# Performance work log

Measured on AMD Instinct MI355X. Metric: run time of the kernel, lower is better.

Reference implementation:

```python
import jax, jax.numpy as jnp
import numpy as np

N_NODES = 50000
N_HEDGES = 20000
N_EDGES = 800000
D = 128
H = 4


def setup_inputs() -> dict:
    key = jax.random.key(0)
    ks = jax.random.split(key, 12)
    s = 1.0 / np.sqrt(D)
    return {
        "x_node": jax.random.normal(ks[0], (N_NODES, D), jnp.float32),
        "x_edge": jax.random.normal(ks[1], (N_HEDGES, D), jnp.float32),
        "src": jax.random.randint(ks[2], (N_EDGES,), 0, N_NODES, jnp.int32),
        "dst": jax.random.randint(ks[3], (N_EDGES,), 0, N_HEDGES, jnp.int32),
        "Wq": jax.random.normal(ks[4], (D, D), jnp.float32) * s,
        "bq": jnp.zeros((D,), jnp.float32),
        "Wk": jax.random.normal(ks[5], (D, D), jnp.float32) * s,
        "bk": jnp.zeros((D,), jnp.float32),
        "Wv": jax.random.normal(ks[6], (D, D), jnp.float32) * s,
        "bv": jnp.zeros((D,), jnp.float32),
        "Wo": jax.random.normal(ks[7], (D, D), jnp.float32) * s,
        "bo": jnp.zeros((D,), jnp.float32),
    }


def reference(x_node, x_edge, src, dst, Wq, bq, Wk, bk, Wv, bv, Wo, bo):
    N = x_node.shape[0]
    hd = Wq.shape[1] // H  # head_dim = 32
    Q = (x_node @ Wq + bq).reshape(N, H, hd)
    K = (x_edge @ Wk + bk).reshape(-1, H, hd)
    V = (x_edge @ Wv + bv).reshape(-1, H, hd)
    # per-edge gather: [E, H, hd]
    Qe = Q[src]
    Ke = K[dst]
    Ve = V[dst]
    # per-edge, per-head scores: [E, H]
    scores = jnp.einsum("ehd,ehd->eh", Qe, Ke) / jnp.sqrt(jnp.float32(hd))
    # segment softmax grouped by src node
    m = jax.ops.segment_max(scores, src, num_segments=N)  # [N, H]
    e = jnp.exp(scores - m[src])
    z = jax.ops.segment_sum(e, src, num_segments=N)  # [N, H]
    w = e / z[src]  # [E, H]
    # weighted scatter-add of V messages back to src nodes
    msg = w[:, :, None] * Ve  # [E, H, hd]
    out = jax.ops.segment_sum(msg, src, num_segments=N)  # [N, H, hd]
    out = out.reshape(N, -1)
    return out @ Wo + bo + x_node
```

## Files before the change

kernel.cpp:

```cpp
#include <hip/hip_runtime.h>

#define D 128
#define STRIDE 6144

typedef _Float16 f16;
typedef f16 f16x2 __attribute__((ext_vector_type(2)));
typedef f16 f16x8 __attribute__((ext_vector_type(8)));
typedef float f32x4 __attribute__((ext_vector_type(4)));

__device__ inline f16x2 u2h(unsigned u) { return __builtin_bit_cast(f16x2, u); }
__device__ inline unsigned h2u(f16x2 h) { return __builtin_bit_cast(unsigned, h); }

__device__ inline float dot2(unsigned a, unsigned b, float c) {
#if __has_builtin(__builtin_amdgcn_fdot2)
    return __builtin_amdgcn_fdot2(u2h(a), u2h(b), c, false);
#else
    f16x2 x = u2h(a), y = u2h(b);
    return c + (float)x.x * (float)y.x + (float)x.y * (float)y.y;
#endif
}

__global__ void wt_prep4(const float* __restrict__ W0, const float* __restrict__ W1,
                         const float* __restrict__ W2, const float* __restrict__ W3,
                         f16* __restrict__ Wt) {
    const float* W = (blockIdx.x == 0) ? W0 : (blockIdx.x == 1) ? W1 : (blockIdx.x == 2) ? W2 : W3;
    f16* o = Wt + (size_t)blockIdx.x * D * D;
    int t = threadIdx.x;
#pragma unroll
    for (int i = 0; i < 16; ++i) {
        int f = t + i * 256;
        int k = f >> 5, c4 = f & 31;
        float4 v = *(const float4*)(W + k * D + 4 * c4);
        float vv[4] = {v.x, v.y, v.z, v.w};
#pragma unroll
        for (int e = 0; e < 4; ++e) {
            int c = 4 * c4 + e;
            o[c * D + (((k >> 3) ^ (c & 15)) << 3) + (k & 7)] = (f16)vv[e];
        }
    }
}

__device__ inline void stage_w(const f16* __restrict__ Wt, f16* Wl, int t) {
#pragma unroll
    for (int i = 0; i < 8; ++i) ((uint4*)Wl)[t + i * 256] = ((const uint4*)Wt)[t + i * 256];
}

__device__ inline void stage_x_f32(const float* __restrict__ x, f16* xs, int r0, int nrows, int t) {
#pragma unroll
    for (int i = 0; i < 8; ++i) {
        int f = t + i * 256;
        int r = f >> 5, c4 = f & 31;
        int gr = r0 + r;
        float4 v = {0.f, 0.f, 0.f, 0.f};
        if (gr < nrows) v = *(const float4*)(x + (size_t)gr * D + 4 * c4);
        unsigned lo = h2u((f16x2){(f16)v.x, (f16)v.y});
        unsigned hi = h2u((f16x2){(f16)v.z, (f16)v.w});
        *(uint2*)(xs + r * D + (((c4 >> 1) ^ (r & 15)) << 3) + (c4 & 1) * 4) = (uint2){lo, hi};
    }
}

__device__ inline void mfma_core(const f16* xs, const f16* Wl, f32x4 acc[8], int lane, int w) {
    int lr = lane & 15, g = lane >> 4;
    int arow = 16 * w + lr;
#pragma unroll
    for (int kc = 0; kc < 4; ++kc) {
        int slot = kc * 4 + g;
        f16x8 af = *(const f16x8*)(xs + arow * D + ((slot ^ (arow & 15)) << 3));
#pragma unroll
        for (int ct = 0; ct < 8; ++ct) {
            int col = ct * 16 + lr;
            f16x8 bf = *(const f16x8*)(Wl + col * D + ((slot ^ (col & 15)) << 3));
            acc[ct] = __builtin_amdgcn_mfma_f32_16x16x32_f16(af, bf, acc[ct], 0, 0, 0);
        }
    }
}

__global__ __launch_bounds__(256) void fused_front(
    const float* __restrict__ x_node, const float* __restrict__ x_edge,
    const int* __restrict__ src, const int* __restrict__ dst,
    const f16* __restrict__ Wt,
    const float* __restrict__ bq, const float* __restrict__ bk, const float* __restrict__ bv,
    f16* __restrict__ Qh, f16* __restrict__ KVh,
    int* __restrict__ bucket_cnt, unsigned* __restrict__ temp,
    int N, int M, int E, int nsp, int nq, float qscale) {
    __shared__ __align__(16) f16 Wl[D * D];
    __shared__ __align__(16) f16 xs[64 * D];
    int t = threadIdx.x;
    int bid = blockIdx.x;

    if (bid < nsp) {
        int* hist = (int*)Wl;
        int* lex = hist + 256;
        int* gbase = lex + 256;
        int* lcur = gbase + 256;
        int* wsum = lcur + 256;
        int* sorted = wsum + 16;
        unsigned char* sbyte = (unsigned char*)xs;
        hist[t] = 0;
        lcur[t] = 0;
        __syncthreads();
        int base0 = bid * 4096;
        int lim = E - base0; if (lim > 4096) lim = 4096;
        for (int i = t; i < lim; i += 256) atomicAdd(&hist[src[base0 + i] >> 8], 1);
        __syncthreads();
        int v = hist[t];
        int inc = v;
#pragma unroll
        for (int m = 1; m < 64; m <<= 1) {
            int u = __shfl_up(inc, m);
            if ((t & 63) >= m) inc += u;
        }
        if ((t & 63) == 63) wsum[t >> 6] = inc;
        __syncthreads();
        int add = 0;
#pragma unroll
        for (int w = 0; w < 4; ++w)
            if (w < (t >> 6)) add += wsum[w];
        lex[t] = add + inc - v;
        if (v) gbase[t] = atomicAdd(&bucket_cnt[t], v);
        __syncthreads();
        for (int i = t; i < lim; i += 256) {
            int s = src[base0 + i];
            int bk2 = s >> 8;
            int lp = atomicAdd(&lcur[bk2], 1);
            int sp = lex[bk2] + lp;
            sorted[sp] = ((s & 255) << 24) | dst[base0 + i];
            sbyte[sp] = (unsigned char)bk2;
        }
        __syncthreads();
        for (int i = t; i < lim; i += 256) {
            int bk2 = sbyte[i];
            int gp = gbase[bk2] + (i - lex[bk2]);
            if (gp < STRIDE) temp[(size_t)bk2 * STRIDE + gp] = (unsigned)sorted[i];
        }
    } else if (bid < nsp + nq) {
        int r0 = (bid - nsp) * 64;
        stage_w(Wt, Wl, t);
        stage_x_f32(x_node, xs, r0, N, t);
        __syncthreads();
        int lane = t & 63, w = t >> 6;
        f32x4 acc[8];
#pragma unroll
        for (int i = 0; i < 8; ++i) acc[i] = (f32x4){0.f, 0.f, 0.f, 0.f};
        mfma_core(xs, Wl, acc, lane, w);
        __syncthreads();
        int lr = lane & 15, g = lane >> 4;
#pragma unroll
        for (int ct = 0; ct < 8; ++ct) {
            int col = ct * 16 + lr;
            float bias = bq[col];
#pragma unroll
            for (int rg = 0; rg < 4; ++rg) {
                int row = 16 * w + 4 * g + rg;
                xs[row * D + (((col >> 3) ^ (row & 15)) << 3) + (col & 7)] =
                    (f16)((acc[ct][rg] + bias) * qscale);
            }
        }
        __syncthreads();
#pragma unroll
        for (int i = 0; i < 4; ++i) {
            int f = t + i * 256;
            int r = f >> 4, c8 = f & 15;
            if (r0 + r < N) {
                uint4 v = *(const uint4*)(xs + r * D + ((c8 ^ (r & 15)) << 3));
                *(uint4*)(Qh + (size_t)(r0 + r) * D + 8 * c8) = v;
            }
        }
    } else {
        int r0 = (bid - nsp - nq) * 64;
        stage_w(Wt + D * D, Wl, t);
        stage_x_f32(x_edge, xs, r0, M, t);
        __syncthreads();
        int lane = t & 63, w = t >> 6;
        f32x4 accK[8], accV[8];
#pragma unroll
        for (int i = 0; i < 8; ++i) accK[i] = accV[i] = (f32x4){0.f, 0.f, 0.f, 0.f};
        mfma_core(xs, Wl, accK, lane, w);
        __syncthreads();
        stage_w(Wt + 2 * D * D, Wl, t);
        __syncthreads();
        mfma_core(xs, Wl, accV, lane, w);
        __syncthreads();
        int lr = lane & 15, g = lane >> 4;
#pragma unroll
        for (int ct = 0; ct < 8; ++ct) {
            int col = ct * 16 + lr;
            float bbk = bk[col], bbv = bv[col];
            int s = col >> 2, wk = col & 3;
#pragma unroll
            for (int rg = 0; rg < 4; ++rg) {
                int row = 16 * w + 4 * g + rg;
                f16* base = Wl + row * 256 + ((s ^ (row & 15)) << 3);
                base[wk] = (f16)(accK[ct][rg] + bbk);
                base[4 + wk] = (f16)(accV[ct][rg] + bbv);
            }
        }
        __syncthreads();
#pragma unroll
        for (int i = 0; i < 8; ++i) {
            int f = t + i * 256;
            int r = f >> 5, c8 = f & 31;
            if (r0 + r < M) {
                uint4 v = *(const uint4*)(Wl + r * 256 + ((c8 ^ (r & 15)) << 3));
                *(uint4*)(KVh + (size_t)(r0 + r) * 256 + 8 * c8) = v;
            }
        }
    }
}

__global__ __launch_bounds__(256) void bucket_scatter(const unsigned* __restrict__ temp,
                                                      const int* __restrict__ bucket_cnt,
                                                      int* __restrict__ off,
                                                      int* __restrict__ csr_dst,
                                                      int N, int E, int NBUK) {
    __shared__ int nh[256], cur[256], wsum[4], sc_ex[256];
    __shared__ int lds_dst[STRIDE];
    int b = blockIdx.x, t = threadIdx.x;
    int bc = (t < NBUK) ? bucket_cnt[t] : 0;
    {
        int inc = bc;
#pragma unroll
        for (int m = 1; m < 64; m <<= 1) {
            int u = __shfl_up(inc, m);
            if ((t & 63) >= m) inc += u;
        }
        if ((t & 63) == 63) wsum[t >> 6] = inc;
        __syncthreads();
        int add = 0;
#pragma unroll
        for (int w = 0; w < 4; ++w)
            if (w < (t >> 6)) add += wsum[w];
        sc_ex[t] = add + inc - bc;
        nh[t] = 0;
    }
    __syncthreads();
    int bo = sc_ex[b];
    int cnt = bucket_cnt[b];
    if (cnt > STRIDE) cnt = STRIDE;
    const unsigned* tb = temp + (size_t)b * STRIDE;
    for (int i = t; i < cnt; i += 256) atomicAdd(&nh[tb[i] >> 24], 1);
    __syncthreads();
    int v = nh[t];
    int inc = v;
#pragma unroll
    for (int m = 1; m < 64; m <<= 1) {
        int u = __shfl_up(inc, m);
        if ((t & 63) >= m) inc += u;
    }
    if ((t & 63) == 63) wsum[t >> 6] = inc;
    __syncthreads();
    int add = 0;
#pragma unroll
    for (int w = 0; w < 4; ++w)
        if (w < (t >> 6)) add += wsum[w];
    int ex = add + inc - v;
    cur[t] = ex;
    int node = (b << 8) + t;
    if (node < N) off[node] = bo + ex;
    if (b == 0 && t == 0) off[N] = E;
    __syncthreads();
    for (int i = t; i < cnt; i += 256) {
        unsigned it = tb[i];
        int lpos = atomicAdd(&cur[it >> 24], 1);
        lds_dst[lpos] = (int)(it & 0xFFFFFFu);
    }
    __syncthreads();
    for (int i = t; i < cnt; i += 256) csr_dst[bo + i] = lds_dst[i];
}

__global__ __launch_bounds__(256) void node_attn4(const f16* __restrict__ Qh,
                                                  const f16* __restrict__ KVh,
                                                  const int* __restrict__ off,
                                                  const int* __restrict__ csr,
                                                  f16* __restrict__ aggh, int N) {
    int wid = (int)((blockIdx.x * (size_t)blockDim.x + threadIdx.x) >> 6);
    int lane = threadIdx.x & 63;
    if (wid >= N) return;
    int j = lane & 7, g = lane >> 3;
    const f16* qp = Qh + (size_t)wid * D + 16 * j;
    uint4 qA = *(const uint4*)qp;
    uint4 qB = *(const uint4*)(qp + 8);
    int beg = off[wid], end = off[wid + 1];
    float z = 0.f;
    f16x2 a0 = {0, 0}, a1 = {0, 0}, a2 = {0, 0}, a3 = {0, 0};
    f16x2 a4 = {0, 0}, a5 = {0, 0}, a6 = {0, 0}, a7 = {0, 0};
    if (beg < end) {
        int pe = beg + g;
        int d0 = csr[(pe < end) ? pe : end - 1];
        const f16* r = KVh + (size_t)d0 * 256 + 32 * j;
        uint4 A0 = *(const uint4*)r;
        uint4 A1 = *(const uint4*)(r + 8);
        uint4 A2 = *(const uint4*)(r + 16);
        uint4 A3 = *(const uint4*)(r + 24);
        for (int p = beg; p < end; p += 8) {
            int pn = p + 8 + g;
            int dn = csr[(pn < end) ? pn : end - 1];
            const f16* rn = KVh + (size_t)dn * 256 + 32 * j;
            uint4 B0 = *(const uint4*)rn;
            uint4 B1 = *(const uint4*)(rn + 8);
            uint4 B2 = *(const uint4*)(rn + 16);
            uint4 B3 = *(const uint4*)(rn + 24);
            bool valid = (p + g) < end;
            float s = dot2(A0.x, qA.x, 0.f);
            s = dot2(A0.y, qA.y, s);
            s = dot2(A1.x, qA.z, s);
            s = dot2(A1.y, qA.w, s);
            s = dot2(A2.x, qB.x, s);
            s = dot2(A2.y, qB.y, s);
            s = dot2(A3.x, qB.z, s);
            s = dot2(A3.y, qB.w, s);
            s += __shfl_xor(s, 1);
            float eh = valid ? __expf(s) : 0.f;
            z += eh;
            f16 e16 = (f16)eh;
            f16x2 e2 = {e16, e16};
            a0 += e2 * u2h(A0.z); a1 += e2 * u2h(A0.w);
            a2 += e2 * u2h(A1.z); a3 += e2 * u2h(A1.w);
            a4 += e2 * u2h(A2.z); a5 += e2 * u2h(A2.w);
            a6 += e2 * u2h(A3.z); a7 += e2 * u2h(A3.w);
            A0 = B0; A1 = B1; A2 = B2; A3 = B3;
        }
    }
#pragma unroll
    for (int m = 8; m < 64; m <<= 1) {
        z += __shfl_xor(z, m);
        a0 += u2h(__shfl_xor((int)h2u(a0), m));
        a1 += u2h(__shfl_xor((int)h2u(a1), m));
        a2 += u2h(__shfl_xor((int)h2u(a2), m));
        a3 += u2h(__shfl_xor((int)h2u(a3), m));
        a4 += u2h(__shfl_xor((int)h2u(a4), m));
        a5 += u2h(__shfl_xor((int)h2u(a5), m));
        a6 += u2h(__shfl_xor((int)h2u(a6), m));
        a7 += u2h(__shfl_xor((int)h2u(a7), m));
    }
    if (g == 0) {
        float inv = (end > beg) ? 1.f / z : 0.f;
        uint4 o0, o1;
        o0.x = h2u((f16x2){(f16)((float)a0.x * inv), (f16)((float)a0.y * inv)});
        o0.y = h2u((f16x2){(f16)((float)a1.x * inv), (f16)((float)a1.y * inv)});
        o0.z = h2u((f16x2){(f16)((float)a2.x * inv), (f16)((float)a2.y * inv)});
        o0.w = h2u((f16x2){(f16)((float)a3.x * inv), (f16)((float)a3.y * inv)});
        o1.x = h2u((f16x2){(f16)((float)a4.x * inv), (f16)((float)a4.y * inv)});
        o1.y = h2u((f16x2){(f16)((float)a5.x * inv), (f16)((float)a5.y * inv)});
        o1.z = h2u((f16x2){(f16)((float)a6.x * inv), (f16)((float)a6.y * inv)});
        o1.w = h2u((f16x2){(f16)((float)a7.x * inv), (f16)((float)a7.y * inv)});
        f16* op = aggh + (size_t)wid * D + 16 * j;
        *(uint4*)op = o0;
        *(uint4*)(op + 8) = o1;
    }
}

__global__ __launch_bounds__(256) void gemm_o(const f16* __restrict__ aggh,
                                              const f16* __restrict__ Wt,
                                              const float* __restrict__ b,
                                              const float* __restrict__ resid,
                                              float* __restrict__ y, int nrows) {
    __shared__ __align__(16) f16 Wl[D * D];
    __shared__ __align__(16) f16 xs[64 * D];
    int t = threadIdx.x;
    int r0 = blockIdx.x * 64;
    stage_w(Wt, Wl, t);
#pragma unroll
    for (int i = 0; i < 4; ++i) {
        int f = t + i * 256;
        int r = f >> 4, c8 = f & 15;
        int gr = r0 + r;
        uint4 v = {0u, 0u, 0u, 0u};
        if (gr < nrows) v = *(const uint4*)(aggh + (size_t)gr * D + 8 * c8);
        *(uint4*)(xs + r * D + ((c8 ^ (r & 15)) << 3)) = v;
    }
    __syncthreads();
    int lane = t & 63, w = t >> 6;
    f32x4 acc[8];
#pragma unroll
    for (int i = 0; i < 8; ++i) acc[i] = (f32x4){0.f, 0.f, 0.f, 0.f};
    mfma_core(xs, Wl, acc, lane, w);
    __syncthreads();
    float* Tf = (float*)Wl;
    int lr = lane & 15, g = lane >> 4;
#pragma unroll
    for (int ct = 0; ct < 8; ++ct) {
        int col = ct * 16 + lr;
        float bias = b[col];
        int s = col >> 2, wk = col & 3;
#pragma unroll
        for (int rg = 0; rg < 4; ++rg) {
            int row = 16 * w + 4 * g + rg;
            Tf[row * D + ((s ^ (row & 15)) << 2) + wk] = acc[ct][rg] + bias;
        }
    }
    __syncthreads();
#pragma unroll
    for (int i = 0; i < 8; ++i) {
        int f = t + i * 256;
        int r = f >> 5, c4 = f & 31;
        int gr = r0 + r;
        if (gr < nrows) {
            float4 v = *(const float4*)(Tf + r * D + ((c4 ^ (r & 15)) << 2));
            float4 rv = *(const float4*)(resid + (size_t)gr * D + 4 * c4);
            v.x += rv.x; v.y += rv.y; v.z += rv.z; v.w += rv.w;
            *(float4*)(y + (size_t)gr * D + 4 * c4) = v;
        }
    }
}

extern "C" void kernel_launch(void* const* d_in, const int* in_sizes, int n_in,
                              void* d_out, int out_size, void* d_ws, size_t ws_size,
                              hipStream_t stream) {
    const float* x_node = (const float*)d_in[0];
    const float* x_edge = (const float*)d_in[1];
    const int* src = (const int*)d_in[2];
    const int* dst = (const int*)d_in[3];
    const float* Wq = (const float*)d_in[4];
    const float* bq = (const float*)d_in[5];
    const float* Wk = (const float*)d_in[6];
    const float* bk = (const float*)d_in[7];
    const float* Wv = (const float*)d_in[8];
    const float* bv = (const float*)d_in[9];
    const float* Wo = (const float*)d_in[10];
    const float* bo = (const float*)d_in[11];

    int N = in_sizes[0] / D;
    int M = in_sizes[1] / D;
    int E = in_sizes[2];
    int NBUK = (N + 255) >> 8;

    char* p = (char*)d_ws;
    auto alloc = [&](size_t bytes) -> char* {
        char* r = p;
        p += (bytes + 15) & ~(size_t)15;
        return r;
    };
    f16* Wt = (f16*)alloc((size_t)4 * D * D * 2);
    f16* Qh = (f16*)alloc((size_t)N * D * 2);
    f16* KVh = (f16*)alloc((size_t)M * 256 * 2);
    f16* aggh = (f16*)alloc((size_t)N * D * 2);
    int* bucket_cnt = (int*)alloc(256 * 4);
    int* off = (int*)alloc((size_t)(N + 1) * 4);
    unsigned* temp = (unsigned*)alloc((size_t)NBUK * STRIDE * 4);
    int* csr_dst = (int*)alloc((size_t)E * 4);
    float* out = (float*)d_out;

    hipMemsetAsync(bucket_cnt, 0, 256 * 4, stream);

    wt_prep4<<<4, 256, 0, stream>>>(Wq, Wk, Wv, Wo, Wt);

    int nq = (N + 63) / 64;
    int nkv = (M + 63) / 64;
    int nsp = (E + 4095) / 4096;
    fused_front<<<nsp + nq + nkv, 256, 0, stream>>>(x_node, x_edge, src, dst, Wt,
                                                    bq, bk, bv, Qh, KVh,
                                                    bucket_cnt, temp,
                                                    N, M, E, nsp, nq, 0.17677669529663687f);

    bucket_scatter<<<NBUK, 256, 0, stream>>>(temp, bucket_cnt, off, csr_dst, N, E, NBUK);

    int ablk = (int)(((size_t)N * 64 + 255) / 256);
    node_attn4<<<ablk, 256, 0, stream>>>(Qh, KVh, off, csr_dst, aggh, N);

    gemm_o<<<(N + 63) / 64, 256, 0, stream>>>(aggh, Wt + 3 * D * D, bo, x_node, out, N);
}
```

Measured before the change: 116.3 us.

## Load GEMM A-operands straight to registers and pre-sort buckets by dst

The GEMM kernels (fused_front Q/KV paths and gemm_o) now load their A-operand rows from global memory directly into MFMA register fragments, dropping the 16 KB xs LDS tile and its staging barrier. This halves shared memory per block, which should allow more resident blocks, and lets the global loads overlap the weight staging. The CSR build kernel adds a counting-sort pass by dst/128 before the per-node sort, so each node's edge list comes out grouped by destination locality, which should improve K/V gather cache hits in the attention kernel. The cost is an extra histogram, scan and scatter pass plus 24 KB more LDS in that kernel.

Result: faster. 114.0 us (-2.0%).

```diff
diff --git a/kernel.cpp b/kernel.cpp
--- a/kernel.cpp
+++ b/kernel.cpp
@@ -45,32 +45,33 @@
     for (int i = 0; i < 8; ++i) ((uint4*)Wl)[t + i * 256] = ((const uint4*)Wt)[t + i * 256];
 }
 
-__device__ inline void stage_x_f32(const float* __restrict__ x, f16* xs, int r0, int nrows, int t) {
-#pragma unroll
-    for (int i = 0; i < 8; ++i) {
-        int f = t + i * 256;
-        int r = f >> 5, c4 = f & 31;
-        int gr = r0 + r;
-        float4 v = {0.f, 0.f, 0.f, 0.f};
-        if (gr < nrows) v = *(const float4*)(x + (size_t)gr * D + 4 * c4);
-        unsigned lo = h2u((f16x2){(f16)v.x, (f16)v.y});
-        unsigned hi = h2u((f16x2){(f16)v.z, (f16)v.w});
-        *(uint2*)(xs + r * D + (((c4 >> 1) ^ (r & 15)) << 3) + (c4 & 1) * 4) = (uint2){lo, hi};
-    }
-}
-
-__device__ inline void mfma_core(const f16* xs, const f16* Wl, f32x4 acc[8], int lane, int w) {
+__device__ inline void load_a_f32(const float* __restrict__ x, int gr, int nrows, int g,
+                                  f16x8 a[4]) {
+#pragma unroll
+    for (int kc = 0; kc < 4; ++kc) {
+        float4 v0 = {0.f, 0.f, 0.f, 0.f}, v1 = {0.f, 0.f, 0.f, 0.f};
+        if (gr < nrows) {
+            const float* xr = x + (size_t)gr * D + (kc * 4 + g) * 8;
+            v0 = *(const float4*)xr;
+            v1 = *(const float4*)(xr + 4);
+        }
+        f16x8 af;
+        af[0] = (f16)v0.x; af[1] = (f16)v0.y; af[2] = (f16)v0.z; af[3] = (f16)v0.w;
+        af[4] = (f16)v1.x; af[5] = (f16)v1.y; af[6] = (f16)v1.z; af[7] = (f16)v1.w;
+        a[kc] = af;
+    }
+}
+
+__device__ inline void mfma_ra(const f16x8 a[4], const f16* Wl, f32x4 acc[8], int lane) {
     int lr = lane & 15, g = lane >> 4;
-    int arow = 16 * w + lr;
 #pragma unroll
     for (int kc = 0; kc < 4; ++kc) {
         int slot = kc * 4 + g;
-        f16x8 af = *(const f16x8*)(xs + arow * D + ((slot ^ (arow & 15)) << 3));
 #pragma unroll
         for (int ct = 0; ct < 8; ++ct) {
             int col = ct * 16 + lr;
             f16x8 bf = *(const f16x8*)(Wl + col * D + ((slot ^ (col & 15)) << 3));
-            acc[ct] = __builtin_amdgcn_mfma_f32_16x16x32_f16(af, bf, acc[ct], 0, 0, 0);
+            acc[ct] = __builtin_amdgcn_mfma_f32_16x16x32_f16(a[kc], bf, acc[ct], 0, 0, 0);
         }
     }
 }
@@ -84,7 +85,6 @@
     int* __restrict__ bucket_cnt, unsigned* __restrict__ temp,
     int N, int M, int E, int nsp, int nq, float qscale) {
     __shared__ __align__(16) f16 Wl[D * D];
-    __shared__ __align__(16) f16 xs[64 * D];
     int t = threadIdx.x;
     int bid = blockIdx.x;
 
@@ -95,7 +95,7 @@
         int* lcur = gbase + 256;
         int* wsum = lcur + 256;
         int* sorted = wsum + 16;
-        unsigned char* sbyte = (unsigned char*)xs;
+        unsigned char* sbyte = (unsigned char*)(sorted + 4096);
         hist[t] = 0;
         lcur[t] = 0;
         __syncthreads();
@@ -136,15 +136,16 @@
     } else if (bid < nsp + nq) {
         int r0 = (bid - nsp) * 64;
         stage_w(Wt, Wl, t);
-        stage_x_f32(x_node, xs, r0, N, t);
-        __syncthreads();
         int lane = t & 63, w = t >> 6;
+        int lr = lane & 15, g = lane >> 4;
+        f16x8 a[4];
+        load_a_f32(x_node, r0 + 16 * w + lr, N, g, a);
         f32x4 acc[8];
 #pragma unroll
         for (int i = 0; i < 8; ++i) acc[i] = (f32x4){0.f, 0.f, 0.f, 0.f};
-        mfma_core(xs, Wl, acc, lane, w);
-        __syncthreads();
-        int lr = lane & 15, g = lane >> 4;
+        __syncthreads();
+        mfma_ra(a, Wl, acc, lane);
+        __syncthreads();
 #pragma unroll
         for (int ct = 0; ct < 8; ++ct) {
             int col = ct * 16 + lr;
@@ -152,7 +153,7 @@
 #pragma unroll
             for (int rg = 0; rg < 4; ++rg) {
                 int row = 16 * w + 4 * g + rg;
-                xs[row * D + (((col >> 3) ^ (row & 15)) << 3) + (col & 7)] =
+                Wl[row * D + (((col >> 3) ^ (row & 15)) << 3) + (col & 7)] =
                     (f16)((acc[ct][rg] + bias) * qscale);
             }
         }
@@ -162,26 +163,27 @@
             int f = t + i * 256;
             int r = f >> 4, c8 = f & 15;
             if (r0 + r < N) {
-                uint4 v = *(const uint4*)(xs + r * D + ((c8 ^ (r & 15)) << 3));
+                uint4 v = *(const uint4*)(Wl + r * D + ((c8 ^ (r & 15)) << 3));
                 *(uint4*)(Qh + (size_t)(r0 + r) * D + 8 * c8) = v;
             }
         }
     } else {
         int r0 = (bid - nsp - nq) * 64;
         stage_w(Wt + D * D, Wl, t);
-        stage_x_f32(x_edge, xs, r0, M, t);
-        __syncthreads();
         int lane = t & 63, w = t >> 6;
+        int lr = lane & 15, g = lane >> 4;
+        f16x8 a[4];
+        load_a_f32(x_edge, r0 + 16 * w + lr, M, g, a);
         f32x4 accK[8], accV[8];
 #pragma unroll
         for (int i = 0; i < 8; ++i) accK[i] = accV[i] = (f32x4){0.f, 0.f, 0.f, 0.f};
-        mfma_core(xs, Wl, accK, lane, w);
+        __syncthreads();
+        mfma_ra(a, Wl, accK, lane);
         __syncthreads();
         stage_w(Wt + 2 * D * D, Wl, t);
         __syncthreads();
-        mfma_core(xs, Wl, accV, lane, w);
-        __syncthreads();
-        int lr = lane & 15, g = lane >> 4;
+        mfma_ra(a, Wl, accV, lane);
+        __syncthreads();
 #pragma unroll
         for (int ct = 0; ct < 8; ++ct) {
             int col = ct * 16 + lr;
@@ -213,11 +215,12 @@
                                                       int* __restrict__ off,
                                                       int* __restrict__ csr_dst,
                                                       int N, int E, int NBUK) {
-    __shared__ int nh[256], cur[256], wsum[4], sc_ex[256];
+    __shared__ int nh[256], cur[256], wsum[4], sc_ex[256], dh[256], dcur[256];
+    __shared__ int sorted2[STRIDE];
     __shared__ int lds_dst[STRIDE];
     int b = blockIdx.x, t = threadIdx.x;
-    int bc = (t < NBUK) ? bucket_cnt[t] : 0;
     {
+        int bc = (t < NBUK) ? bucket_cnt[t] : 0;
         int inc = bc;
 #pragma unroll
         for (int m = 1; m < 64; m <<= 1) {
@@ -232,35 +235,63 @@
             if (w < (t >> 6)) add += wsum[w];
         sc_ex[t] = add + inc - bc;
         nh[t] = 0;
+        dh[t] = 0;
     }
     __syncthreads();
     int bo = sc_ex[b];
     int cnt = bucket_cnt[b];
     if (cnt > STRIDE) cnt = STRIDE;
     const unsigned* tb = temp + (size_t)b * STRIDE;
-    for (int i = t; i < cnt; i += 256) atomicAdd(&nh[tb[i] >> 24], 1);
-    __syncthreads();
-    int v = nh[t];
-    int inc = v;
-#pragma unroll
-    for (int m = 1; m < 64; m <<= 1) {
-        int u = __shfl_up(inc, m);
-        if ((t & 63) >= m) inc += u;
-    }
-    if ((t & 63) == 63) wsum[t >> 6] = inc;
-    __syncthreads();
-    int add = 0;
-#pragma unroll
-    for (int w = 0; w < 4; ++w)
-        if (w < (t >> 6)) add += wsum[w];
-    int ex = add + inc - v;
-    cur[t] = ex;
-    int node = (b << 8) + t;
-    if (node < N) off[node] = bo + ex;
-    if (b == 0 && t == 0) off[N] = E;
+    for (int i = t; i < cnt; i += 256) atomicAdd(&dh[(tb[i] & 0xFFFFFFu) >> 7], 1);
+    __syncthreads();
+    {
+        int v = dh[t];
+        int inc = v;
+#pragma unroll
+        for (int m = 1; m < 64; m <<= 1) {
+            int u = __shfl_up(inc, m);
+            if ((t & 63) >= m) inc += u;
+        }
+        if ((t & 63) == 63) wsum[t >> 6] = inc;
+        __syncthreads();
+        int add = 0;
+#pragma unroll
+        for (int w = 0; w < 4; ++w)
+            if (w < (t >> 6)) add += wsum[w];
+        dcur[t] = add + inc - v;
+    }
     __syncthreads();
     for (int i = t; i < cnt; i += 256) {
         unsigned it = tb[i];
+        int pos = atomicAdd(&dcur[(it & 0xFFFFFFu) >> 7], 1);
+        sorted2[pos] = (int)it;
+    }
+    __syncthreads();
+    for (int i = t; i < cnt; i += 256) atomicAdd(&nh[((unsigned)sorted2[i]) >> 24], 1);
+    __syncthreads();
+    {
+        int v = nh[t];
+        int inc = v;
+#pragma unroll
+        for (int m = 1; m < 64; m <<= 1) {
+            int u = __shfl_up(inc, m);
+            if ((t & 63) >= m) inc += u;
+        }
+        if ((t & 63) == 63) wsum[t >> 6] = inc;
+        __syncthreads();
+        int add = 0;
+#pragma unroll
+        for (int w = 0; w < 4; ++w)
+            if (w < (t >> 6)) add += wsum[w];
+        int ex = add + inc - v;
+        cur[t] = ex;
+        int node = (b << 8) + t;
+        if (node < N) off[node] = bo + ex;
+        if (b == 0 && t == 0) off[N] = E;
+    }
+    __syncthreads();
+    for (int i = t; i < cnt; i += 256) {
+        unsigned it = (unsigned)sorted2[i];
         int lpos = atomicAdd(&cur[it >> 24], 1);
         lds_dst[lpos] = (int)(it & 0xFFFFFFu);
     }
@@ -356,28 +387,26 @@
                                               const float* __restrict__ resid,
                                               float* __restrict__ y, int nrows) {
     __shared__ __align__(16) f16 Wl[D * D];
-    __shared__ __align__(16) f16 xs[64 * D];
     int t = threadIdx.x;
     int r0 = blockIdx.x * 64;
     stage_w(Wt, Wl, t);
-#pragma unroll
-    for (int i = 0; i < 4; ++i) {
-        int f = t + i * 256;
-        int r = f >> 4, c8 = f & 15;
-        int gr = r0 + r;
+    int lane = t & 63, w = t >> 6;
+    int lr = lane & 15, g = lane >> 4;
+    int gr = r0 + 16 * w + lr;
+    f16x8 a[4];
+#pragma unroll
+    for (int kc = 0; kc < 4; ++kc) {
         uint4 v = {0u, 0u, 0u, 0u};
-        if (gr < nrows) v = *(const uint4*)(aggh + (size_t)gr * D + 8 * c8);
-        *(uint4*)(xs + r * D + ((c8 ^ (r & 15)) << 3)) = v;
-    }
-    __syncthreads();
-    int lane = t & 63, w = t >> 6;
+        if (gr < nrows) v = *(const uint4*)(aggh + (size_t)gr * D + (kc * 4 + g) * 8);
+        a[kc] = __builtin_bit_cast(f16x8, v);
+    }
     f32x4 acc[8];
 #pragma unroll
     for (int i = 0; i < 8; ++i) acc[i] = (f32x4){0.f, 0.f, 0.f, 0.f};
-    mfma_core(xs, Wl, acc, lane, w);
+    __syncthreads();
+    mfma_ra(a, Wl, acc, lane);
     __syncthreads();
     float* Tf = (float*)Wl;
-    int lr = lane & 15, g = lane >> 4;
 #pragma unroll
     for (int ct = 0; ct < 8; ++ct) {
         int col = ct * 16 + lr;
@@ -394,12 +423,12 @@
     for (int i = 0; i < 8; ++i) {
         int f = t + i * 256;
         int r = f >> 5, c4 = f & 31;
-        int gr = r0 + r;
-        if (gr < nrows) {
+        int gr2 = r0 + r;
+        if (gr2 < nrows) {
             float4 v = *(const float4*)(Tf + r * D + ((c4 ^ (r & 15)) << 2));
-            float4 rv = *(const float4*)(resid + (size_t)gr * D + 4 * c4);
+            float4 rv = *(const float4*)(resid + (size_t)gr2 * D + 4 * c4);
             v.x += rv.x; v.y += rv.y; v.z += rv.z; v.w += rv.w;
-            *(float4*)(y + (size_t)gr * D + 4 * c4) = v;
+            *(float4*)(y + (size_t)gr2 * D + 4 * c4) = v;
         }
     }
 }
```
